# Performance work log

Hardware: AMD Instinct MI355X
Metric: run time of the kernel (lower is better)

Reference implementation:

```python
import jax, jax.numpy as jnp
import numpy as np

WINDOW_SIZE = 7
NUM_HEADS = 6
DIM = 192
HEAD_DIM = DIM // NUM_HEADS


def _relative_position_index(ws: int) -> np.ndarray:
    coords = np.stack(np.meshgrid(np.arange(ws), np.arange(ws), indexing='ij'))  # [2, ws, ws]
    coords = coords.reshape(2, -1)  # [2, ws*ws]
    rel = coords[:, :, None] - coords[:, None, :]  # [2, N, N]
    rel = rel.transpose(1, 2, 0).astype(np.int64)  # [N, N, 2]
    rel[..., 0] += ws - 1
    rel[..., 1] += ws - 1
    rel[..., 0] *= 2 * ws - 1
    return rel.sum(-1)  # [N, N] in [0, (2*ws-1)^2)


def setup_inputs() -> dict:
    key = jax.random.key(0)
    ks = jax.random.split(key, 6)
    B, N, C = 8192, WINDOW_SIZE * WINDOW_SIZE, DIM
    return {
        'x': jax.random.normal(ks[0], (B, N, C), dtype=jnp.float32),
        'qkv_w': jax.random.normal(ks[1], (3 * C, C), dtype=jnp.float32) * 0.02,
        'qkv_b': jax.random.normal(ks[2], (3 * C,), dtype=jnp.float32) * 0.02,
        'proj_w': jax.random.normal(ks[3], (C, C), dtype=jnp.float32) * 0.02,
        'proj_b': jax.random.normal(ks[4], (C,), dtype=jnp.float32) * 0.02,
        'bias_table': jax.random.normal(ks[5], ((2 * WINDOW_SIZE - 1) ** 2, NUM_HEADS), dtype=jnp.float32) * 0.02,
    }


def reference(x, qkv_w, qkv_b, proj_w, proj_b, bias_table):
    B, N, C = x.shape
    H, hd = NUM_HEADS, HEAD_DIM
    scale = hd ** -0.5
    rel_idx = jnp.asarray(_relative_position_index(WINDOW_SIZE))  # [N, N] static

    qkv = x @ qkv_w.T + qkv_b  # [B, N, 3C]
    qkv = qkv.reshape(B, N, 3, H, hd).transpose(2, 0, 3, 1, 4)  # [3, B, H, N, hd]
    q, k, v = qkv[0], qkv[1], qkv[2]

    attn = jnp.einsum('bhnd,bhmd->bhnm', q * scale, k)  # [B, H, N, N]
    bias = bias_table[rel_idx]  # [N, N, H]
    attn = attn + bias.transpose(2, 0, 1)[None]  # broadcast over B
    attn = jax.nn.softmax(attn, axis=-1)

    out = jnp.einsum('bhnm,bhmd->bhnd', attn, v)  # [B, H, N, hd]
    out = out.transpose(0, 2, 1, 3).reshape(B, N, C)
    return out @ proj_w.T + proj_b
```

## Files before the change

kernel.cpp:

```cpp
#include <hip/hip_runtime.h>
#include <hip/hip_bf16.h>
#include <cstdint>
#include <cstddef>

typedef float  f32x4 __attribute__((ext_vector_type(4)));
typedef short  s16x8 __attribute__((ext_vector_type(8)));

#define NTOK   49
#define CDIM   192
#define HEADS  6
#define SCALE  0.17677669529663689f
#define LOG2E  1.4426950408889634f

#define WS_BIAS_BYTES  98304
#define WS_WQ_BYTES    221184
#define WS_TOTAL_BYTES (WS_BIAS_BYTES + WS_WQ_BYTES + 73728)

static __device__ __forceinline__ ushort f2bf(float f) {
  __hip_bfloat16 h = __float2bfloat16(f);
  union { __hip_bfloat16 h; ushort u; } c; c.h = h;
  return c.u;
}

static __device__ __forceinline__ s16x8 pack8(f32x4 a, f32x4 b) {
  union { s16x8 v; __hip_bfloat162 h[4]; } u;
  u.h[0] = __float22bfloat162_rn(make_float2(a[0], a[1]));
  u.h[1] = __float22bfloat162_rn(make_float2(a[2], a[3]));
  u.h[2] = __float22bfloat162_rn(make_float2(b[0], b[1]));
  u.h[3] = __float22bfloat162_rn(make_float2(b[2], b[3]));
  return u.v;
}

static __device__ __forceinline__ f32x4 mfma_bf16(s16x8 a, s16x8 b, f32x4 c) {
  return __builtin_amdgcn_mfma_f32_16x16x32_bf16(a, b, c, 0, 0, 0);
}

__global__ void wconv_kernel(const float* __restrict__ qkv_w,
                             const float* __restrict__ proj_w,
                             const float* __restrict__ bias_table,
                             ushort* __restrict__ wqs, ushort* __restrict__ wps,
                             float* __restrict__ biasT) {
  int i = blockIdx.x * 256 + threadIdx.x;
  if (i < 576 * 192) {
    int n = i / 192, k = i % 192;
    int dst = ((n >> 4) * 6 + (k >> 5)) * 512 + ((k >> 3) & 3) * 128 + (n & 15) * 8 + (k & 7);
    wqs[dst] = f2bf(qkv_w[i]);
  }
  if (i < 192 * 192) {
    int n = i / 192, k = i % 192;
    int dst = ((n >> 4) * 6 + (k >> 5)) * 512 + ((k >> 3) & 3) * 128 + (n & 15) * 8 + (k & 7);
    wps[dst] = f2bf(proj_w[i]);
  }
  if (i < HEADS * 4096) {
    int h = i >> 12, r = i & 4095;
    int lane = (r >> 2) & 63, e = r & 3;
    int qt = r >> 10, kt = (r >> 8) & 3;
    int q   = qt * 16 + (lane & 15);
    int key = kt * 16 + (lane >> 4) * 4 + e;
    float v;
    if (key >= NTOK)      v = -1e30f;
    else if (q >= NTOK)   v = 0.f;
    else {
      int qd = q / 7, qm = q % 7, kd = key / 7, km = key % 7;
      int ri = (qd - kd + 6) * 13 + (qm - km + 6);
      v = bias_table[ri * 6 + h];
    }
    biasT[i] = v;
  }
}

template <bool WB>
__global__ __launch_bounds__(768, 3)
void wattn_kernel(const float* __restrict__ x,
                  const float* __restrict__ qkv_w, const float* __restrict__ qkv_b,
                  const float* __restrict__ proj_w, const float* __restrict__ proj_b,
                  const float* __restrict__ bias_table,
                  const ushort* __restrict__ wqs, const ushort* __restrict__ wps,
                  const float* __restrict__ biasT,
                  float* __restrict__ out, int nwin) {
  __shared__ __align__(16) ushort XB[2][64 * 200];
  __shared__ __align__(16) float  BL[WB ? 4 : 1024];

  const int tid  = threadIdx.x;
  const int lane = tid & 63;
  const int wv   = tid >> 6;
  const int winl = wv / 6;
  const int w    = wv - winl * 6;
  const int l16  = lane & 15;
  const int lk   = lane >> 4;
  const int win  = blockIdx.x * 2 + winl;
  const int h    = w;

#pragma unroll
  for (int it = 0; it < 8; ++it) {
    int v = tid + it * 768;
    int wl2 = v / 3072, r = v - wl2 * 3072;
    int row = r / 48, c4 = r - row * 48;
    int wgl = blockIdx.x * 2 + wl2;
    float4 f = {0.f, 0.f, 0.f, 0.f};
    if (row < NTOK && wgl < nwin)
      f = *(const float4*)(x + (size_t)wgl * (NTOK * CDIM) + row * CDIM + c4 * 4);
    union { ushort4 u; __hip_bfloat162 h[2]; } cc;
    cc.h[0] = __float22bfloat162_rn(make_float2(f.x, f.y));
    cc.h[1] = __float22bfloat162_rn(make_float2(f.z, f.w));
    *(ushort4*)&XB[wl2][row * 200 + c4 * 4] = cc.u;
  }
  if constexpr (!WB) {
    for (int v = tid; v < 169 * 6; v += 768) BL[v] = bias_table[v];
  }
  __syncthreads();

  s16x8 bq[4], ak[4], bv[2][2];

  {
    f32x4 acc[4][2] = {};
#pragma unroll
    for (int ks = 0; ks < 6; ++ks) {
      const int k0 = ks * 32 + lk * 8;
      s16x8 xa[4];
#pragma unroll
      for (int mt = 0; mt < 4; ++mt)
        xa[mt] = *(const s16x8*)&XB[winl][(mt * 16 + l16) * 200 + k0];
#pragma unroll
      for (int nt2 = 0; nt2 < 2; ++nt2) {
        s16x8 wf;
        if constexpr (WB) {
          wf = *(const s16x8*)&wqs[(((2 * 12 + w * 2 + nt2) * 6 + ks) << 9) + lk * 128 + l16 * 8];
        } else {
          const float* p = qkv_w + (2 * 192 + w * 32 + nt2 * 16 + l16) * 192 + k0;
          float4 f0 = *(const float4*)p, f1 = *(const float4*)(p + 4);
          f32x4 a = {f0.x,f0.y,f0.z,f0.w}, b = {f1.x,f1.y,f1.z,f1.w}; wf = pack8(a, b);
        }
#pragma unroll
        for (int mt = 0; mt < 4; ++mt)
          acc[mt][nt2] = mfma_bf16(xa[mt], wf, acc[mt][nt2]);
      }
    }
#pragma unroll
    for (int nd = 0; nd < 2; ++nd) {
      const float vb = qkv_b[2 * 192 + w * 32 + nd * 16 + l16];
      f32x4 v0 = acc[0][nd], v1 = acc[1][nd], v2 = acc[2][nd], v3 = acc[3][nd];
#pragma unroll
      for (int i = 0; i < 4; ++i) { v0[i]+=vb; v1[i]+=vb; v2[i]+=vb; v3[i]+=vb; }
      bv[nd][0] = pack8(v0, v1);
      bv[nd][1] = pack8(v2, v3);
    }
  }

  {
    f32x4 acc[2][4] = {};
#pragma unroll
    for (int ks = 0; ks < 6; ++ks) {
      const int k0 = ks * 32 + lk * 8;
      s16x8 xa[4];
#pragma unroll
      for (int mt = 0; mt < 4; ++mt)
        xa[mt] = *(const s16x8*)&XB[winl][(mt * 16 + l16) * 200 + k0];
#pragma unroll
      for (int nt2 = 0; nt2 < 2; ++nt2) {
        s16x8 wf;
        if constexpr (WB) {
          wf = *(const s16x8*)&wqs[(((0 * 12 + w * 2 + nt2) * 6 + ks) << 9) + lk * 128 + l16 * 8];
        } else {
          const float* p = qkv_w + (0 * 192 + w * 32 + nt2 * 16 + l16) * 192 + k0;
          float4 f0 = *(const float4*)p, f1 = *(const float4*)(p + 4);
          f32x4 a = {f0.x,f0.y,f0.z,f0.w}, b = {f1.x,f1.y,f1.z,f1.w}; wf = pack8(a, b);
        }
#pragma unroll
        for (int mt = 0; mt < 4; ++mt)
          acc[nt2][mt] = mfma_bf16(wf, xa[mt], acc[nt2][mt]);
      }
    }
    const float4 b0 = *(const float4*)&qkv_b[0 * 192 + w * 32 +  0 + lk * 4];
    const float4 b1 = *(const float4*)&qkv_b[0 * 192 + w * 32 + 16 + lk * 4];
#pragma unroll
    for (int t = 0; t < 4; ++t) {
      f32x4 a0 = acc[0][t], a1 = acc[1][t];
      a0[0]=(a0[0]+b0.x)*SCALE; a0[1]=(a0[1]+b0.y)*SCALE; a0[2]=(a0[2]+b0.z)*SCALE; a0[3]=(a0[3]+b0.w)*SCALE;
      a1[0]=(a1[0]+b1.x)*SCALE; a1[1]=(a1[1]+b1.y)*SCALE; a1[2]=(a1[2]+b1.z)*SCALE; a1[3]=(a1[3]+b1.w)*SCALE;
      bq[t] = pack8(a0, a1);
    }
  }

  {
    f32x4 acc[2][4] = {};
#pragma unroll
    for (int ks = 0; ks < 6; ++ks) {
      const int k0 = ks * 32 + lk * 8;
      s16x8 xa[4];
#pragma unroll
      for (int mt = 0; mt < 4; ++mt)
        xa[mt] = *(const s16x8*)&XB[winl][(mt * 16 + l16) * 200 + k0];
#pragma unroll
      for (int nt2 = 0; nt2 < 2; ++nt2) {
        s16x8 wf;
        if constexpr (WB) {
          wf = *(const s16x8*)&wqs[(((1 * 12 + w * 2 + nt2) * 6 + ks) << 9) + lk * 128 + l16 * 8];
        } else {
          const float* p = qkv_w + (1 * 192 + w * 32 + nt2 * 16 + l16) * 192 + k0;
          float4 f0 = *(const float4*)p, f1 = *(const float4*)(p + 4);
          f32x4 a = {f0.x,f0.y,f0.z,f0.w}, b = {f1.x,f1.y,f1.z,f1.w}; wf = pack8(a, b);
        }
#pragma unroll
        for (int mt = 0; mt < 4; ++mt)
          acc[nt2][mt] = mfma_bf16(wf, xa[mt], acc[nt2][mt]);
      }
    }
    const float4 b0 = *(const float4*)&qkv_b[1 * 192 + w * 32 +  0 + lk * 4];
    const float4 b1 = *(const float4*)&qkv_b[1 * 192 + w * 32 + 16 + lk * 4];
#pragma unroll
    for (int t = 0; t < 4; ++t) {
      f32x4 a0 = acc[0][t], a1 = acc[1][t];
      a0[0]+=b0.x; a0[1]+=b0.y; a0[2]+=b0.z; a0[3]+=b0.w;
      a1[0]+=b1.x; a1[1]+=b1.y; a1[2]+=b1.z; a1[3]+=b1.w;
      ak[t] = pack8(a0, a1);
    }
  }
  __syncthreads();

#pragma unroll
  for (int qt = 0; qt < 4; ++qt) {
    f32x4 s[4];
#pragma unroll
    for (int kt = 0; kt < 4; ++kt) {
      f32x4 z = {0.f, 0.f, 0.f, 0.f};
      s[kt] = mfma_bf16(ak[kt], bq[qt], z);
    }
    float mx = -1e30f;
    if constexpr (WB) {
#pragma unroll
      for (int kt = 0; kt < 4; ++kt) {
        f32x4 b4 = *(const f32x4*)&biasT[h * 4096 + qt * 1024 + kt * 256 + lane * 4];
#pragma unroll
        for (int i = 0; i < 4; ++i) {
          float sv = s[kt][i] + b4[i];
          s[kt][i] = sv;
          mx = fmaxf(mx, sv);
        }
      }
    } else {
      const int q  = qt * 16 + l16;
      const int qd = q / 7, qm = q % 7;
#pragma unroll
      for (int kt = 0; kt < 4; ++kt)
#pragma unroll
        for (int i = 0; i < 4; ++i) {
          const int key = kt * 16 + lk * 4 + i;
          float sv = s[kt][i];
          if (key < NTOK) {
            int kd = key / 7, km = key % 7;
            int ri = (qd - kd + 6) * 13 + (qm - km + 6);
            ri = ri < 0 ? 0 : (ri > 168 ? 168 : ri);
            sv += BL[ri * 6 + h];
          } else sv = -1e30f;
          s[kt][i] = sv;
          mx = fmaxf(mx, sv);
        }
    }
    mx = fmaxf(mx, __shfl_xor(mx, 16));
    mx = fmaxf(mx, __shfl_xor(mx, 32));
    float sum = 0.f;
#pragma unroll
    for (int kt = 0; kt < 4; ++kt)
#pragma unroll
      for (int i = 0; i < 4; ++i) {
        float p = exp2f((s[kt][i] - mx) * LOG2E);
        s[kt][i] = p; sum += p;
      }
    sum += __shfl_xor(sum, 16);
    sum += __shfl_xor(sum, 32);
    const float rinv = 1.f / sum;
#pragma unroll
    for (int kt = 0; kt < 4; ++kt)
#pragma unroll
      for (int i = 0; i < 4; ++i) s[kt][i] *= rinv;

    s16x8 pa0 = pack8(s[0], s[1]);
    s16x8 pa1 = pack8(s[2], s[3]);
#pragma unroll
    for (int nd = 0; nd < 2; ++nd) {
      f32x4 z = {0.f, 0.f, 0.f, 0.f};
      f32x4 o = mfma_bf16(pa0, bv[nd][0], z);
      o = mfma_bf16(pa1, bv[nd][1], o);
#pragma unroll
      for (int i = 0; i < 4; ++i)
        XB[winl][(qt * 16 + lk * 4 + i) * 200 + h * 32 + nd * 16 + l16] = f2bf(o[i]);
    }
  }
  __syncthreads();

  {
    f32x4 pc[4][2] = {};
#pragma unroll
    for (int ks = 0; ks < 6; ++ks) {
      const int k0 = ks * 32 + lk * 8;
      s16x8 a[4];
#pragma unroll
      for (int mt = 0; mt < 4; ++mt)
        a[mt] = *(const s16x8*)&XB[winl][(mt * 16 + l16) * 200 + k0];
#pragma unroll
      for (int nt = 0; nt < 2; ++nt) {
        s16x8 b;
        if constexpr (WB) {
          b = *(const s16x8*)&wps[(((w * 2 + nt) * 6 + ks) << 9) + lk * 128 + l16 * 8];
        } else {
          const int n = w * 32 + nt * 16 + l16;
          const float* p = proj_w + n * 192 + k0;
          float4 f0 = *(const float4*)p, f1 = *(const float4*)(p + 4);
          f32x4 fa = {f0.x,f0.y,f0.z,f0.w}, fb = {f1.x,f1.y,f1.z,f1.w};
          b = pack8(fa, fb);
        }
#pragma unroll
        for (int mt = 0; mt < 4; ++mt)
          pc[mt][nt] = mfma_bf16(a[mt], b, pc[mt][nt]);
      }
    }
    if (win < nwin) {
#pragma unroll
      for (int nt = 0; nt < 2; ++nt) {
        const int n = w * 32 + nt * 16 + l16;
        const float pbias = proj_b[n];
#pragma unroll
        for (int mt = 0; mt < 4; ++mt)
#pragma unroll
          for (int i = 0; i < 4; ++i) {
            const int row = mt * 16 + lk * 4 + i;
            if (row < NTOK)
              out[((size_t)win * NTOK + row) * CDIM + n] = pc[mt][nt][i] + pbias;
          }
      }
    }
  }
}

extern "C" void kernel_launch(void* const* d_in, const int* in_sizes, int n_in,
                              void* d_out, int out_size, void* d_ws, size_t ws_size,
                              hipStream_t stream) {
  const float* x          = (const float*)d_in[0];
  const float* qkv_w      = (const float*)d_in[1];
  const float* qkv_b      = (const float*)d_in[2];
  const float* proj_w     = (const float*)d_in[3];
  const float* proj_b     = (const float*)d_in[4];
  const float* bias_table = (const float*)d_in[5];
  float* out = (float*)d_out;

  const int nwin   = in_sizes[0] / (NTOK * CDIM);
  const int nblk   = (nwin + 1) / 2;

  if (ws_size >= WS_TOTAL_BYTES) {
    float*  biasT = (float*)d_ws;
    ushort* wqs   = (ushort*)((char*)d_ws + WS_BIAS_BYTES);
    ushort* wps   = (ushort*)((char*)d_ws + WS_BIAS_BYTES + WS_WQ_BYTES);
    wconv_kernel<<<dim3(432), dim3(256), 0, stream>>>(qkv_w, proj_w, bias_table, wqs, wps, biasT);
    wattn_kernel<true><<<dim3(nblk), dim3(768), 0, stream>>>(
        x, qkv_w, qkv_b, proj_w, proj_b, bias_table, wqs, wps, biasT, out, nwin);
  } else {
    wattn_kernel<false><<<dim3(nblk), dim3(768), 0, stream>>>(
        x, qkv_w, qkv_b, proj_w, proj_b, bias_table, nullptr, nullptr, nullptr, out, nwin);
  }
}
```

Baseline: 421.7 us.

## Stage K and V fragments in shared memory instead of registers

K and V projection results are now written to new per-window LDS buffers and reloaded with volatile 64-bit reads right before each attention MFMA, instead of staying live in registers across the Q projection. The K bias add is dropped, which relies on softmax being invariant to the per-query constant q·bk. The aim is to cut VGPR pressure during the projection and attention phases. The cost is about 96 KB of extra LDS per block, which likely cuts the number of resident blocks per CU well below the launch-bounds target of three. It also adds LDS traffic and volatile loads that the compiler cannot schedule freely.

```diff
diff --git a/kernel.cpp b/kernel.cpp
--- a/kernel.cpp
+++ b/kernel.cpp
@@ -19,6 +19,13 @@
 static __device__ __forceinline__ ushort f2bf(float f) {
   __hip_bfloat16 h = __float2bfloat16(f);
   union { __hip_bfloat16 h; ushort u; } c; c.h = h;
+  return c.u;
+}
+
+static __device__ __forceinline__ ushort4 pack4(f32x4 a) {
+  union { ushort4 u; __hip_bfloat162 h[2]; } c;
+  c.h[0] = __float22bfloat162_rn(make_float2(a[0], a[1]));
+  c.h[1] = __float22bfloat162_rn(make_float2(a[2], a[3]));
   return c.u;
 }
 
@@ -79,6 +86,8 @@
                   const float* __restrict__ biasT,
                   float* __restrict__ out, int nwin) {
   __shared__ __align__(16) ushort XB[2][64 * 200];
+  __shared__ __align__(16) ushort KS[2][HEADS * 2048];
+  __shared__ __align__(16) ushort VT[2][HEADS * 2048];
   __shared__ __align__(16) float  BL[WB ? 4 : 1024];
 
   const int tid  = threadIdx.x;
@@ -110,7 +119,7 @@
   }
   __syncthreads();
 
-  s16x8 bq[4], ak[4], bv[2][2];
+  s16x8 bq[4];
 
   {
     f32x4 acc[4][2] = {};
@@ -137,14 +146,46 @@
       }
     }
 #pragma unroll
-    for (int nd = 0; nd < 2; ++nd) {
-      const float vb = qkv_b[2 * 192 + w * 32 + nd * 16 + l16];
-      f32x4 v0 = acc[0][nd], v1 = acc[1][nd], v2 = acc[2][nd], v3 = acc[3][nd];
-#pragma unroll
-      for (int i = 0; i < 4; ++i) { v0[i]+=vb; v1[i]+=vb; v2[i]+=vb; v3[i]+=vb; }
-      bv[nd][0] = pack8(v0, v1);
-      bv[nd][1] = pack8(v2, v3);
-    }
+    for (int nt2 = 0; nt2 < 2; ++nt2) {
+      const float vb = qkv_b[2 * 192 + w * 32 + nt2 * 16 + l16];
+#pragma unroll
+      for (int mt = 0; mt < 4; ++mt) {
+        f32x4 a = acc[mt][nt2];
+        a[0] += vb; a[1] += vb; a[2] += vb; a[3] += vb;
+        *(ushort4*)&VT[winl][((w * 8 + nt2 * 4 + mt) * 64 + lane) * 4] = pack4(a);
+      }
+    }
+  }
+
+  {
+    f32x4 acc[2][4] = {};
+#pragma unroll
+    for (int ks = 0; ks < 6; ++ks) {
+      const int k0 = ks * 32 + lk * 8;
+      s16x8 xa[4];
+#pragma unroll
+      for (int mt = 0; mt < 4; ++mt)
+        xa[mt] = *(const s16x8*)&XB[winl][(mt * 16 + l16) * 200 + k0];
+#pragma unroll
+      for (int nt2 = 0; nt2 < 2; ++nt2) {
+        s16x8 wf;
+        if constexpr (WB) {
+          wf = *(const s16x8*)&wqs[(((1 * 12 + w * 2 + nt2) * 6 + ks) << 9) + lk * 128 + l16 * 8];
+        } else {
+          const float* p = qkv_w + (1 * 192 + w * 32 + nt2 * 16 + l16) * 192 + k0;
+          float4 f0 = *(const float4*)p, f1 = *(const float4*)(p + 4);
+          f32x4 a = {f0.x,f0.y,f0.z,f0.w}, b = {f1.x,f1.y,f1.z,f1.w}; wf = pack8(a, b);
+        }
+#pragma unroll
+        for (int mt = 0; mt < 4; ++mt)
+          acc[nt2][mt] = mfma_bf16(wf, xa[mt], acc[nt2][mt]);
+      }
+    }
+#pragma unroll
+    for (int nt2 = 0; nt2 < 2; ++nt2)
+#pragma unroll
+      for (int mt = 0; mt < 4; ++mt)
+        *(ushort4*)&KS[winl][((w * 8 + mt * 2 + nt2) * 64 + lane) * 4] = pack4(acc[nt2][mt]);
   }
 
   {
@@ -181,41 +222,6 @@
       bq[t] = pack8(a0, a1);
     }
   }
-
-  {
-    f32x4 acc[2][4] = {};
-#pragma unroll
-    for (int ks = 0; ks < 6; ++ks) {
-      const int k0 = ks * 32 + lk * 8;
-      s16x8 xa[4];
-#pragma unroll
-      for (int mt = 0; mt < 4; ++mt)
-        xa[mt] = *(const s16x8*)&XB[winl][(mt * 16 + l16) * 200 + k0];
-#pragma unroll
-      for (int nt2 = 0; nt2 < 2; ++nt2) {
-        s16x8 wf;
-        if constexpr (WB) {
-          wf = *(const s16x8*)&wqs[(((1 * 12 + w * 2 + nt2) * 6 + ks) << 9) + lk * 128 + l16 * 8];
-        } else {
-          const float* p = qkv_w + (1 * 192 + w * 32 + nt2 * 16 + l16) * 192 + k0;
-          float4 f0 = *(const float4*)p, f1 = *(const float4*)(p + 4);
-          f32x4 a = {f0.x,f0.y,f0.z,f0.w}, b = {f1.x,f1.y,f1.z,f1.w}; wf = pack8(a, b);
-        }
-#pragma unroll
-        for (int mt = 0; mt < 4; ++mt)
-          acc[nt2][mt] = mfma_bf16(wf, xa[mt], acc[nt2][mt]);
-      }
-    }
-    const float4 b0 = *(const float4*)&qkv_b[1 * 192 + w * 32 +  0 + lk * 4];
-    const float4 b1 = *(const float4*)&qkv_b[1 * 192 + w * 32 + 16 + lk * 4];
-#pragma unroll
-    for (int t = 0; t < 4; ++t) {
-      f32x4 a0 = acc[0][t], a1 = acc[1][t];
-      a0[0]+=b0.x; a0[1]+=b0.y; a0[2]+=b0.z; a0[3]+=b0.w;
-      a1[0]+=b1.x; a1[1]+=b1.y; a1[2]+=b1.z; a1[3]+=b1.w;
-      ak[t] = pack8(a0, a1);
-    }
-  }
   __syncthreads();
 
 #pragma unroll
@@ -223,8 +229,11 @@
     f32x4 s[4];
 #pragma unroll
     for (int kt = 0; kt < 4; ++kt) {
+      union { s16x8 v; uint64_t q[2]; } akc;
+      akc.q[0] = *(const volatile uint64_t*)&KS[winl][((w * 8 + kt * 2 + 0) * 64 + lane) * 4];
+      akc.q[1] = *(const volatile uint64_t*)&KS[winl][((w * 8 + kt * 2 + 1) * 64 + lane) * 4];
       f32x4 z = {0.f, 0.f, 0.f, 0.f};
-      s[kt] = mfma_bf16(ak[kt], bq[qt], z);
+      s[kt] = mfma_bf16(akc.v, bq[qt], z);
     }
     float mx = -1e30f;
     if constexpr (WB) {
@@ -279,9 +288,14 @@
     s16x8 pa1 = pack8(s[2], s[3]);
 #pragma unroll
     for (int nd = 0; nd < 2; ++nd) {
+      union { s16x8 v; uint64_t q[2]; } b0c, b1c;
+      b0c.q[0] = *(const volatile uint64_t*)&VT[winl][((w * 8 + nd * 4 + 0) * 64 + lane) * 4];
+      b0c.q[1] = *(const volatile uint64_t*)&VT[winl][((w * 8 + nd * 4 + 1) * 64 + lane) * 4];
+      b1c.q[0] = *(const volatile uint64_t*)&VT[winl][((w * 8 + nd * 4 + 2) * 64 + lane) * 4];
+      b1c.q[1] = *(const volatile uint64_t*)&VT[winl][((w * 8 + nd * 4 + 3) * 64 + lane) * 4];
       f32x4 z = {0.f, 0.f, 0.f, 0.f};
-      f32x4 o = mfma_bf16(pa0, bv[nd][0], z);
-      o = mfma_bf16(pa1, bv[nd][1], o);
+      f32x4 o = mfma_bf16(pa0, b0c.v, z);
+      o = mfma_bf16(pa1, b1c.v, o);
 #pragma unroll
       for (int i = 0; i < 4; ++i)
         XB[winl][(qt * 16 + lk * 4 + i) * 200 + h * 32 + nd * 16 + l16] = f2bf(o[i]);
@@ -344,8 +358,8 @@
   const float* bias_table = (const float*)d_in[5];
   float* out = (float*)d_out;
 
-  const int nwin   = in_sizes[0] / (NTOK * CDIM);
-  const int nblk   = (nwin + 1) / 2;
+  const int nwin = in_sizes[0] / (NTOK * CDIM);
+  const int nblk = (nwin + 1) / 2;
 
   if (ws_size >= WS_TOTAL_BYTES) {
     float*  biasT = (float*)d_ws;
```

Result: slower. 506.5 us (median of 2 runs) (+20.1%).
